# Kernel tuning notes

Hardware: AMD Instinct MI355X
Metric: run time of the kernel (lower is better)

Reference implementation:

```python
import jax, jax.numpy as jnp
import numpy as np

TEMPERATURE = 1.0
TINY = np.finfo(np.float32).tiny


def setup_inputs() -> dict:
    key = jax.random.key(0)
    ks = jax.random.split(key, 8)
    B, D, H, K, OUT = 2048, 1024, 512, 32, 2
    s = lambda *sh: 1.0 / np.sqrt(sh[0])
    return {
        "x": jax.random.normal(ks[0], (B, D), jnp.float32),
        "uniform": jax.random.uniform(ks[1], (B, K, D), jnp.float32, TINY, 1.0),
        "w0": jax.random.normal(ks[2], (D, H), jnp.float32) * s(D),
        "b0": jnp.zeros((H,), jnp.float32),
        "w1": jax.random.normal(ks[3], (H, H), jnp.float32) * s(H),
        "b1": jnp.zeros((H,), jnp.float32),
        "wout": jax.random.normal(ks[4], (H, D), jnp.float32) * s(H),
        "bout": jnp.zeros((D,), jnp.float32),
        "wp0": jax.random.normal(ks[5], (D, H), jnp.float32) * s(D),
        "bp0": jnp.zeros((H,), jnp.float32),
        "wp1": jax.random.normal(ks[6], (H, OUT), jnp.float32) * s(H),
        "bp1": jnp.zeros((OUT,), jnp.float32),
        "k": K,
    }


def reference(x, uniform, w0, b0, w1, b1, wout, bout, wp0, bp0, wp1, bp1, k):
    # Selector MLP: relu hidden layers, softmax output over the d features.
    h = jax.nn.relu(x @ w0 + b0)
    h = jax.nn.relu(h @ w1 + b1)
    logits = jax.nn.softmax(h @ wout + bout, axis=-1)  # [B, D]

    # create_mask, training branch: Gumbel-softmax concrete relaxation.
    # uniform: [B, K, D]; gumbel = -log(-log(u))
    gumbel = -jnp.log(-jnp.log(uniform))
    noisy = (gumbel + logits[:, None, :]) / TEMPERATURE  # [B, K, D]
    samples = jax.nn.softmax(noisy, axis=-1)
    masks = jnp.max(samples, axis=1)  # [B, D]

    # Predictor MLP on masked inputs (stands in for the saved model).
    new_inputs = x * masks
    hp = jax.nn.relu(new_inputs @ wp0 + bp0)
    deep_out = hp @ wp1 + bp1  # [B, 2]
    return deep_out, masks
```

## Files before the change

kernel.cpp:

```cpp
#include <hip/hip_runtime.h>

#define BB 2048
#define DD 1024
#define HH 512
#define KK 32

#define AS_GLOBAL __attribute__((address_space(1)))
#define AS_LDS    __attribute__((address_space(3)))

typedef __attribute__((ext_vector_type(8))) short short8;
typedef __attribute__((ext_vector_type(4))) float floatx4;

__device__ __forceinline__ float bf2f(unsigned short u) {
    union { unsigned int u; float f; } c; c.u = ((unsigned int)u) << 16; return c.f;
}
__device__ __forceinline__ unsigned short f2bf(float f) {
    union { float f; unsigned int u; } c; c.f = f;
    unsigned int u = c.u + 0x7FFFu + ((c.u >> 16) & 1u);
    return (unsigned short)(u >> 16);
}

#define WOFF_XB    ((size_t)0)
#define WOFF_W0T   ((size_t)4194304)
#define WOFF_W1T   ((size_t)5242880)
#define WOFF_WOUTT ((size_t)5767168)
#define WOFF_WP0T  ((size_t)6815744)
#define WOFF_H0    ((size_t)7864320)
#define WOFF_H1    ((size_t)9961472)
#define WOFF_LG    ((size_t)12058624)
#define WOFF_NEWIN ((size_t)20447232)
#define WOFF_HP    ((size_t)24641536)

__global__ __launch_bounds__(256) void prep_kernel(
    const float* __restrict__ x,  const float* __restrict__ w0,
    const float* __restrict__ w1, const float* __restrict__ wout,
    const float* __restrict__ wp0, unsigned short* __restrict__ ws)
{
    const int blk = blockIdx.x;
    if (blk < 1024) {
        unsigned short* xb = ws + WOFF_XB / 2;
        const size_t base = (size_t)blk * 2048 + (size_t)threadIdx.x * 8;
        float4 v0 = *(const float4*)(x + base);
        float4 v1 = *(const float4*)(x + base + 4);
        ushort4 o0, o1;
        o0.x = f2bf(v0.x); o0.y = f2bf(v0.y); o0.z = f2bf(v0.z); o0.w = f2bf(v0.w);
        o1.x = f2bf(v1.x); o1.y = f2bf(v1.y); o1.z = f2bf(v1.z); o1.w = f2bf(v1.w);
        *(ushort4*)(xb + base) = o0;
        *(ushort4*)(xb + base + 4) = o1;
        return;
    }
    const float* src; unsigned short* dst; int Kd, N, t;
    if (blk < 1536)      { src = w0;   dst = ws + WOFF_W0T / 2;   Kd = 1024; N = 512;  t = blk - 1024; }
    else if (blk < 1792) { src = w1;   dst = ws + WOFF_W1T / 2;   Kd = 512;  N = 512;  t = blk - 1536; }
    else if (blk < 2304) { src = wout; dst = ws + WOFF_WOUTT / 2; Kd = 512;  N = 1024; t = blk - 1792; }
    else                 { src = wp0;  dst = ws + WOFF_WP0T / 2;  Kd = 1024; N = 512;  t = blk - 2304; }
    const int ntn = N / 32;
    const int kt = t / ntn, nt = t % ntn;
    __shared__ float tile[32][33];
    const int tx = threadIdx.x & 31, ty = threadIdx.x >> 5;
#pragma unroll
    for (int r = 0; r < 32; r += 8)
        tile[ty + r][tx] = src[(size_t)(kt * 32 + ty + r) * N + nt * 32 + tx];
    __syncthreads();
#pragma unroll
    for (int r = 0; r < 32; r += 8)
        dst[(size_t)(nt * 32 + ty + r) * Kd + kt * 32 + tx] = f2bf(tile[tx][ty + r]);
}

template <int RELU, int OUTBF>
__global__ __launch_bounds__(256) void gemm_mfma(
    const unsigned short* __restrict__ A,
    const unsigned short* __restrict__ BT,
    const float* __restrict__ bias,
    void* __restrict__ Cv, int M, int N, int Kd)
{
    __shared__ __align__(16) unsigned short As[64 * 32];
    __shared__ __align__(16) unsigned short Bs[64 * 32];
    const int tid = threadIdx.x;
    const int bm = blockIdx.y * 64, bn = blockIdx.x * 64;
    const int wave = tid >> 6, lane = tid & 63;

    floatx4 acc[2][2] = {};

    const int sr = tid >> 2, sc = (tid & 3) * 8;
    const unsigned short* ga = A  + (size_t)(bm + sr) * Kd + sc;
    const unsigned short* gb = BT + (size_t)(bn + sr) * Kd + sc;
    unsigned short* lA = As + (size_t)wave * 512;
    unsigned short* lB = Bs + (size_t)wave * 512;

    const int wm = (wave >> 1) * 32, wn = (wave & 1) * 32;
    const int fr = lane & 15, fk = (lane >> 4) * 8;
    const unsigned short* pa0 = As + (wm + fr) * 32 + fk;
    const unsigned short* pb0 = Bs + (wn + fr) * 32 + fk;

    for (int k0 = 0; k0 < Kd; k0 += 32) {
        __builtin_amdgcn_global_load_lds((const AS_GLOBAL void*)(ga + k0),
                                         (AS_LDS void*)lA, 16, 0, 0);
        __builtin_amdgcn_global_load_lds((const AS_GLOBAL void*)(gb + k0),
                                         (AS_LDS void*)lB, 16, 0, 0);
        __syncthreads();
        short8 a0 = *(const short8*)pa0;
        short8 a1 = *(const short8*)(pa0 + 16 * 32);
        short8 b0 = *(const short8*)pb0;
        short8 b1 = *(const short8*)(pb0 + 16 * 32);
        acc[0][0] = __builtin_amdgcn_mfma_f32_16x16x32_bf16(a0, b0, acc[0][0], 0, 0, 0);
        acc[0][1] = __builtin_amdgcn_mfma_f32_16x16x32_bf16(a0, b1, acc[0][1], 0, 0, 0);
        acc[1][0] = __builtin_amdgcn_mfma_f32_16x16x32_bf16(a1, b0, acc[1][0], 0, 0, 0);
        acc[1][1] = __builtin_amdgcn_mfma_f32_16x16x32_bf16(a1, b1, acc[1][1], 0, 0, 0);
        __syncthreads();
    }

    float* Cf = (float*)Cv;
    unsigned short* Cb = (unsigned short*)Cv;
    const int er = (lane >> 4) * 4, ec = lane & 15;
#pragma unroll
    for (int i = 0; i < 2; ++i)
#pragma unroll
        for (int j = 0; j < 2; ++j) {
            const int col = bn + wn + j * 16 + ec;
            const float bv = bias[col];
#pragma unroll
            for (int r = 0; r < 4; ++r) {
                const int row = bm + wm + i * 16 + er + r;
                float v = acc[i][j][r] + bv;
                if (RELU) v = fmaxf(v, 0.0f);
                if (OUTBF) Cb[(size_t)row * N + col] = f2bf(v);
                else       Cf[(size_t)row * N + col] = v;
            }
        }
}

__device__ __forceinline__ float wave_max(float v) {
#pragma unroll
    for (int o = 32; o; o >>= 1) v = fmaxf(v, __shfl_xor(v, o, 64));
    return v;
}
__device__ __forceinline__ float wave_sum(float v) {
#pragma unroll
    for (int o = 32; o; o >>= 1) v += __shfl_xor(v, o, 64);
    return v;
}

__global__ __launch_bounds__(256) void gumbel_fused(
    const float* __restrict__ lgpre,
    const float* __restrict__ uniform,
    const float* __restrict__ x,
    float* __restrict__ masks,
    unsigned short* __restrict__ newin)
{
    const int wave = threadIdx.x >> 6, lane = threadIdx.x & 63;
    const int b = blockIdx.x * 4 + wave;

    float lp[16];
    const float* lrow = lgpre + (size_t)b * DD;
#pragma unroll
    for (int j = 0; j < 4; ++j)
        *(float4*)(lp + j * 4) = *(const float4*)(lrow + lane * 4 + j * 256);
    float M = -1e30f;
#pragma unroll
    for (int i = 0; i < 16; ++i) M = fmaxf(M, lp[i]);
    M = wave_max(M);
    float S = 0.f;
#pragma unroll
    for (int i = 0; i < 16; ++i) { lp[i] = __expf(lp[i] - M); S += lp[i]; }
    S = wave_sum(S);
    const float invS = 1.0f / S;
    float ep[16];
#pragma unroll
    for (int i = 0; i < 16; ++i) ep[i] = __expf(lp[i] * invS);

    float mk[16] = {0.f,0.f,0.f,0.f,0.f,0.f,0.f,0.f,0.f,0.f,0.f,0.f,0.f,0.f,0.f,0.f};
    const float* up = uniform + (size_t)b * KK * DD;
    for (int k = 0; k < KK; ++k) {
        float sv[16], sloc = 0.f;
#pragma unroll
        for (int j = 0; j < 4; ++j) {
            float4 u4 = *(const float4*)(up + (size_t)k * DD + lane * 4 + j * 256);
            const float uu[4] = {u4.x, u4.y, u4.z, u4.w};
#pragma unroll
            for (int q = 0; q < 4; ++q) {
                const float u = uu[q];
                const float vv = u - 1.0f;
                const float tpoly = -vv * (1.0f + vv * (-0.5f + vv * 0.33333333f));
                const float tlog  = -__logf(u);
                const float t = (u > 0.984375f) ? tpoly : tlog;
                const float s = ep[j * 4 + q] / t;
                sv[j * 4 + q] = s;
                sloc += s;
            }
        }
        const float Sk = wave_sum(sloc);
        const float inv = 1.0f / Sk;
#pragma unroll
        for (int i = 0; i < 16; ++i) mk[i] = fmaxf(mk[i], sv[i] * inv);
    }

#pragma unroll
    for (int j = 0; j < 4; ++j) {
        const int d = lane * 4 + j * 256;
        float4 xv = *(const float4*)(x + (size_t)b * DD + d);
        float4 mo; mo.x = mk[j*4]; mo.y = mk[j*4+1]; mo.z = mk[j*4+2]; mo.w = mk[j*4+3];
        *(float4*)(masks + (size_t)b * DD + d) = mo;
        ushort4 nb;
        nb.x = f2bf(xv.x * mk[j*4]);   nb.y = f2bf(xv.y * mk[j*4+1]);
        nb.z = f2bf(xv.z * mk[j*4+2]); nb.w = f2bf(xv.w * mk[j*4+3]);
        *(ushort4*)(newin + (size_t)b * DD + d) = nb;
    }
}

__global__ __launch_bounds__(256) void final_kernel(
    const unsigned short* __restrict__ hp, const float* __restrict__ wp1,
    const float* __restrict__ bp1, float* __restrict__ out)
{
    const int wave = threadIdx.x >> 6, lane = threadIdx.x & 63;
    const int row = blockIdx.x * 4 + wave;
    const unsigned short* hrow = hp + (size_t)row * HH;
    float a0 = 0.f, a1 = 0.f;
#pragma unroll
    for (int j = 0; j < 8; ++j) {
        const int k = j * 64 + lane;
        const float h = bf2f(hrow[k]);
        const float2 w = *(const float2*)(wp1 + k * 2);
        a0 += h * w.x; a1 += h * w.y;
    }
    a0 = wave_sum(a0); a1 = wave_sum(a1);
    if (lane == 0) {
        out[row * 2 + 0] = a0 + bp1[0];
        out[row * 2 + 1] = a1 + bp1[1];
    }
}

extern "C" void kernel_launch(void* const* d_in, const int* in_sizes, int n_in,
                              void* d_out, int out_size, void* d_ws, size_t ws_size,
                              hipStream_t stream)
{
    (void)in_sizes; (void)n_in; (void)out_size; (void)ws_size;

    const float* x    = (const float*)d_in[0];
    const float* uni  = (const float*)d_in[1];
    const float* w0   = (const float*)d_in[2];
    const float* b0   = (const float*)d_in[3];
    const float* w1   = (const float*)d_in[4];
    const float* b1   = (const float*)d_in[5];
    const float* wout = (const float*)d_in[6];
    const float* bout = (const float*)d_in[7];
    const float* wp0  = (const float*)d_in[8];
    const float* bp0  = (const float*)d_in[9];
    const float* wp1  = (const float*)d_in[10];
    const float* bp1  = (const float*)d_in[11];

    unsigned char* ws = (unsigned char*)d_ws;
    unsigned short* xb    = (unsigned short*)(ws + WOFF_XB);
    unsigned short* w0T   = (unsigned short*)(ws + WOFF_W0T);
    unsigned short* w1T   = (unsigned short*)(ws + WOFF_W1T);
    unsigned short* woutT = (unsigned short*)(ws + WOFF_WOUTT);
    unsigned short* wp0T  = (unsigned short*)(ws + WOFF_WP0T);
    unsigned short* h0    = (unsigned short*)(ws + WOFF_H0);
    unsigned short* h1    = (unsigned short*)(ws + WOFF_H1);
    float*          lg    = (float*)(ws + WOFF_LG);
    unsigned short* newin = (unsigned short*)(ws + WOFF_NEWIN);
    unsigned short* hp    = (unsigned short*)(ws + WOFF_HP);

    float* out   = (float*)d_out;
    float* masks = out + (size_t)BB * 2;

    prep_kernel<<<2816, 256, 0, stream>>>(x, w0, w1, wout, wp0, (unsigned short*)ws);

    gemm_mfma<1, 1><<<dim3(HH / 64, BB / 64), 256, 0, stream>>>(xb, w0T, b0, h0, BB, HH, DD);

    gemm_mfma<1, 1><<<dim3(HH / 64, BB / 64), 256, 0, stream>>>(h0, w1T, b1, h1, BB, HH, HH);

    gemm_mfma<0, 0><<<dim3(DD / 64, BB / 64), 256, 0, stream>>>(h1, woutT, bout, lg, BB, DD, HH);

    gumbel_fused<<<BB / 4, 256, 0, stream>>>(lg, uni, x, masks, newin);

    gemm_mfma<1, 1><<<dim3(HH / 64, BB / 64), 256, 0, stream>>>(newin, wp0T, bp0, hp, BB, HH, DD);

    final_kernel<<<BB / 4, 256, 0, stream>>>(hp, wp1, bp1, out);
}
```

Baseline: 453.8 us.

## Double-buffer swizzled GEMM tiles and use native log2/rcp in Gumbel kernel

The MFMA GEMM now stages 64-wide K tiles into two LDS buffers with an XOR chunk swizzle. The next tile is prefetched while the current one is consumed, leaving one barrier per step instead of two, and bank conflicts on LDS reads should drop. The Gumbel kernel swaps __logf and full division for the native log2 and reciprocal instructions, with the polynomial rescaled by 1/ln2. That constant factor cancels in the softmax normalisation. The trade-offs are slightly lower precision from native rcp and more LDS per block, which may reduce occupancy.

```diff
diff --git a/kernel.cpp b/kernel.cpp
--- a/kernel.cpp
+++ b/kernel.cpp
@@ -74,45 +74,75 @@
     const float* __restrict__ bias,
     void* __restrict__ Cv, int M, int N, int Kd)
 {
-    __shared__ __align__(16) unsigned short As[64 * 32];
-    __shared__ __align__(16) unsigned short Bs[64 * 32];
+    __shared__ __align__(16) unsigned short As[2][4096];
+    __shared__ __align__(16) unsigned short Bs[2][4096];
     const int tid = threadIdx.x;
     const int bm = blockIdx.y * 64, bn = blockIdx.x * 64;
     const int wave = tid >> 6, lane = tid & 63;
 
     floatx4 acc[2][2] = {};
 
-    const int sr = tid >> 2, sc = (tid & 3) * 8;
-    const unsigned short* ga = A  + (size_t)(bm + sr) * Kd + sc;
-    const unsigned short* gb = BT + (size_t)(bn + sr) * Kd + sc;
-    unsigned short* lA = As + (size_t)wave * 512;
-    unsigned short* lB = Bs + (size_t)wave * 512;
+    const int sr = tid >> 3;
+    const int skc = (tid & 7) ^ ((tid >> 3) & 7);
+    const unsigned short* ga = A  + (size_t)(bm + sr) * Kd + skc * 8;
+    const unsigned short* ga2 = ga + (size_t)32 * Kd;
+    const unsigned short* gb = BT + (size_t)(bn + sr) * Kd + skc * 8;
+    const unsigned short* gb2 = gb + (size_t)32 * Kd;
+    const int ldoff = wave * 512;
 
     const int wm = (wave >> 1) * 32, wn = (wave & 1) * 32;
-    const int fr = lane & 15, fk = (lane >> 4) * 8;
-    const unsigned short* pa0 = As + (wm + fr) * 32 + fk;
-    const unsigned short* pb0 = Bs + (wn + fr) * 32 + fk;
-
-    for (int k0 = 0; k0 < Kd; k0 += 32) {
-        __builtin_amdgcn_global_load_lds((const AS_GLOBAL void*)(ga + k0),
-                                         (AS_LDS void*)lA, 16, 0, 0);
-        __builtin_amdgcn_global_load_lds((const AS_GLOBAL void*)(gb + k0),
-                                         (AS_LDS void*)lB, 16, 0, 0);
+    const int fr = lane & 15, fq = lane >> 4;
+    int ua[2], ub[2];
+#pragma unroll
+    for (int i = 0; i < 2; ++i) {
+        const int ra = wm + i * 16 + fr;
+        const int rb = wn + i * 16 + fr;
+        ua[i] = ra * 8;  ub[i] = rb * 8;
+    }
+
+    const int steps = Kd >> 6;
+
+#define STAGE(buf, k0)                                                              \
+    do {                                                                            \
+        __builtin_amdgcn_global_load_lds((const AS_GLOBAL void*)(ga + (k0)),        \
+            (AS_LDS void*)(&As[buf][0] + ldoff), 16, 0, 0);                         \
+        __builtin_amdgcn_global_load_lds((const AS_GLOBAL void*)(ga2 + (k0)),       \
+            (AS_LDS void*)(&As[buf][2048] + ldoff), 16, 0, 0);                      \
+        __builtin_amdgcn_global_load_lds((const AS_GLOBAL void*)(gb + (k0)),        \
+            (AS_LDS void*)(&Bs[buf][0] + ldoff), 16, 0, 0);                         \
+        __builtin_amdgcn_global_load_lds((const AS_GLOBAL void*)(gb2 + (k0)),       \
+            (AS_LDS void*)(&Bs[buf][2048] + ldoff), 16, 0, 0);                      \
+    } while (0)
+
+    STAGE(0, 0);
+    __syncthreads();
+
+    for (int s = 0; s < steps; ++s) {
+        const int buf = s & 1;
+        if (s + 1 < steps) STAGE((s + 1) & 1, (s + 1) << 6);
+#pragma unroll
+        for (int t = 0; t < 2; ++t) {
+            short8 a[2], b[2];
+#pragma unroll
+            for (int i = 0; i < 2; ++i) {
+                const int kc = t * 4 + fq;
+                const int eA = (wm + i * 16 + fr) & 7;
+                const int eB = (wn + i * 16 + fr) & 7;
+                a[i] = *(const short8*)(&As[buf][0] + (size_t)(ua[i] + (kc ^ eA)) * 8);
+                b[i] = *(const short8*)(&Bs[buf][0] + (size_t)(ub[i] + (kc ^ eB)) * 8);
+            }
+            acc[0][0] = __builtin_amdgcn_mfma_f32_16x16x32_bf16(a[0], b[0], acc[0][0], 0, 0, 0);
+            acc[0][1] = __builtin_amdgcn_mfma_f32_16x16x32_bf16(a[0], b[1], acc[0][1], 0, 0, 0);
+            acc[1][0] = __builtin_amdgcn_mfma_f32_16x16x32_bf16(a[1], b[0], acc[1][0], 0, 0, 0);
+            acc[1][1] = __builtin_amdgcn_mfma_f32_16x16x32_bf16(a[1], b[1], acc[1][1], 0, 0, 0);
+        }
         __syncthreads();
-        short8 a0 = *(const short8*)pa0;
-        short8 a1 = *(const short8*)(pa0 + 16 * 32);
-        short8 b0 = *(const short8*)pb0;
-        short8 b1 = *(const short8*)(pb0 + 16 * 32);
-        acc[0][0] = __builtin_amdgcn_mfma_f32_16x16x32_bf16(a0, b0, acc[0][0], 0, 0, 0);
-        acc[0][1] = __builtin_amdgcn_mfma_f32_16x16x32_bf16(a0, b1, acc[0][1], 0, 0, 0);
-        acc[1][0] = __builtin_amdgcn_mfma_f32_16x16x32_bf16(a1, b0, acc[1][0], 0, 0, 0);
-        acc[1][1] = __builtin_amdgcn_mfma_f32_16x16x32_bf16(a1, b1, acc[1][1], 0, 0, 0);
-        __syncthreads();
-    }
+    }
+#undef STAGE
 
     float* Cf = (float*)Cv;
     unsigned short* Cb = (unsigned short*)Cv;
-    const int er = (lane >> 4) * 4, ec = lane & 15;
+    const int er = fq * 4, ec = fr;
 #pragma unroll
     for (int i = 0; i < 2; ++i)
 #pragma unroll
@@ -181,16 +211,16 @@
             for (int q = 0; q < 4; ++q) {
                 const float u = uu[q];
                 const float vv = u - 1.0f;
-                const float tpoly = -vv * (1.0f + vv * (-0.5f + vv * 0.33333333f));
-                const float tlog  = -__logf(u);
+                const float tpoly = -vv * (1.4426950f + vv * (-0.7213475f + vv * 0.4808983f));
+                const float tlog  = -__builtin_amdgcn_logf(u);
                 const float t = (u > 0.984375f) ? tpoly : tlog;
-                const float s = ep[j * 4 + q] / t;
+                const float s = ep[j * 4 + q] * __builtin_amdgcn_rcpf(t);
                 sv[j * 4 + q] = s;
                 sloc += s;
             }
         }
         const float Sk = wave_sum(sloc);
-        const float inv = 1.0f / Sk;
+        const float inv = __builtin_amdgcn_rcpf(Sk);
 #pragma unroll
         for (int i = 0; i < 16; ++i) mk[i] = fmaxf(mk[i], sv[i] * inv);
     }
@@ -267,14 +297,11 @@
     prep_kernel<<<2816, 256, 0, stream>>>(x, w0, w1, wout, wp0, (unsigned short*)ws);
 
     gemm_mfma<1, 1><<<dim3(HH / 64, BB / 64), 256, 0, stream>>>(xb, w0T, b0, h0, BB, HH, DD);
-
     gemm_mfma<1, 1><<<dim3(HH / 64, BB / 64), 256, 0, stream>>>(h0, w1T, b1, h1, BB, HH, HH);
-
     gemm_mfma<0, 0><<<dim3(DD / 64, BB / 64), 256, 0, stream>>>(h1, woutT, bout, lg, BB, DD, HH);
 
     gumbel_fused<<<BB / 4, 256, 0, stream>>>(lg, uni, x, masks, newin);
 
     gemm_mfma<1, 1><<<dim3(HH / 64, BB / 64), 256, 0, stream>>>(newin, wp0T, bp0, hp, BB, HH, DD);
-
     final_kernel<<<BB / 4, 256, 0, stream>>>(hp, wp1, bp1, out);
 }
```

After: 447.1 us. Within noise of the previous version (-1.5%).
